# Kernel optimization log

Measured on AMD Instinct MI355X. Metric: run time of the kernel, lower is better.

Reference implementation:

```python
import jax, jax.numpy as jnp
import numpy as np
import math

N, E, D, H, L = 50000, 800000, 256, 8, 8
DK = D // H
DFF = 4 * D


def _layernorm(h, g, b, eps=1e-5):
    m = jnp.mean(h, axis=-1, keepdims=True)
    v = jnp.mean((h - m) ** 2, axis=-1, keepdims=True)
    return (h - m) * jax.lax.rsqrt(v + eps) * g + b


def setup_inputs() -> dict:
    key = jax.random.key(0)
    ks = jax.random.split(key, 16)
    s = 1.0 / math.sqrt(D)
    x = jax.random.normal(ks[0], (N, D), dtype=jnp.float32)
    # every node gets >=1 in-edge so z > 0 everywhere (as in real connected graphs)
    edge_src = jax.random.randint(ks[1], (E,), 0, N, dtype=jnp.int32)
    edge_dst = jnp.concatenate([
        jnp.arange(N, dtype=jnp.int32),
        jax.random.randint(ks[2], (E - N,), 0, N, dtype=jnp.int32),
    ])
    return {
        "x": x,
        "edge_src": edge_src,
        "edge_dst": edge_dst,
        "Wq": jax.random.normal(ks[3], (L, D, D), dtype=jnp.float32) * s,
        "bq": jnp.zeros((L, D), dtype=jnp.float32),
        "Wk": jax.random.normal(ks[4], (L, D, D), dtype=jnp.float32) * s,
        "Wv": jax.random.normal(ks[5], (L, D, D), dtype=jnp.float32) * s,
        "Wo": jax.random.normal(ks[6], (L, D, D), dtype=jnp.float32) * s,
        "bo": jnp.zeros((L, D), dtype=jnp.float32),
        "ln1_g": jnp.ones((L, D), dtype=jnp.float32),
        "ln1_b": jnp.zeros((L, D), dtype=jnp.float32),
        "W1": jax.random.normal(ks[7], (L, D, DFF), dtype=jnp.float32) * s,
        "b1": jnp.zeros((L, DFF), dtype=jnp.float32),
        "W2": jax.random.normal(ks[8], (L, DFF, D), dtype=jnp.float32) * (1.0 / math.sqrt(DFF)),
        "b2": jnp.zeros((L, D), dtype=jnp.float32),
        "ln2_g": jnp.ones((L, D), dtype=jnp.float32),
        "ln2_b": jnp.zeros((L, D), dtype=jnp.float32),
    }


def _layer(x, src, dst, Wq, bq, Wk, Wv, Wo, bo, g1, b1n, W1, b1, W2, b2, g2, b2n):
    n = x.shape[0]
    q = (x @ Wq + bq).reshape(n, H, DK)
    k = (x @ Wk).reshape(n, H, DK)
    v = (x @ Wv).reshape(n, H, DK)
    # edge score: src_dot_dst('k','q') -> [E, H]
    score = jnp.einsum('ehd,ehd->eh', k[src], q[dst])
    # scaled_exp: exp(clamp(score / sqrt(d_k), -5, 5))
    score = jnp.exp(jnp.clip(score / math.sqrt(DK), -5.0, 5.0))
    # u_mul_e + sum aggregation -> wv [N, H, DK]; copy_edge + sum -> z [N, H]
    msg = v[src] * score[:, :, None]
    wv = jax.ops.segment_sum(msg, dst, num_segments=n)
    z = jax.ops.segment_sum(score, dst, num_segments=n)
    o = (wv / z[:, :, None]).reshape(n, D)
    h = _layernorm(x + o @ Wo + bo, g1, b1n)
    # FFN with residual + layernorm
    ff = jax.nn.relu(h @ W1 + b1) @ W2 + b2
    return _layernorm(h + ff, g2, b2n)


def reference(x, edge_src, edge_dst, Wq, bq, Wk, Wv, Wo, bo, ln1_g, ln1_b,
              W1, b1, W2, b2, ln2_g, ln2_b):
    for i in range(L):
        x = _layer(x, edge_src, edge_dst, Wq[i], bq[i], Wk[i], Wv[i], Wo[i],
                   bo[i], ln1_g[i], ln1_b[i], W1[i], b1[i], W2[i], b2[i],
                   ln2_g[i], ln2_b[i])
    return x
```

## Files before the change

kernel.cpp:

```cpp
#include <hip/hip_runtime.h>
#include <cstdint>
#include <cstddef>

#define D 256
#define H 8
#define DFF 1024

typedef short s16x8 __attribute__((ext_vector_type(8)));
typedef float f32x4 __attribute__((ext_vector_type(4)));

static inline int cdiv(int a, int b) { return (a + b - 1) / b; }

__device__ inline uint16_t f2bf(float x) {
    unsigned u = __float_as_uint(x);
    u += 0x7FFFu + ((u >> 16) & 1u);
    return (uint16_t)(u >> 16);
}
__device__ inline float bf2f(uint16_t h) {
    return __uint_as_float(((unsigned)h) << 16);
}

__device__ inline void gload_lds16(const void* g, void* l) {
    __builtin_amdgcn_global_load_lds(
        (const __attribute__((address_space(1))) void*)g,
        (__attribute__((address_space(3))) void*)l, 16, 0, 0);
}

__global__ __launch_bounds__(256) void zero_int_kernel(int* __restrict__ p, int count)
{
    int i = blockIdx.x * blockDim.x + threadIdx.x;
    if (i < count) p[i] = 0;
}

__global__ __launch_bounds__(256) void count_deg_kernel(
    const int* __restrict__ edst, int* __restrict__ deg, int E)
{
    int e = blockIdx.x * blockDim.x + threadIdx.x;
    if (e < E) atomicAdd(&deg[edst[e]], 1);
}

__global__ __launch_bounds__(256) void block_sum_kernel(
    const int* __restrict__ deg, int* __restrict__ bsum, int N)
{
    int t = threadIdx.x;
    int gid = blockIdx.x * 256 + t;
    int val = (gid < N) ? deg[gid] : 0;
    #pragma unroll
    for (int o = 1; o < 64; o <<= 1) val += __shfl_xor(val, o);
    __shared__ int r[4];
    if ((t & 63) == 0) r[t >> 6] = val;
    __syncthreads();
    if (t == 0) bsum[blockIdx.x] = r[0] + r[1] + r[2] + r[3];
}

__global__ __launch_bounds__(256) void scan_bsum_kernel(int* __restrict__ bsum, int nb)
{
    __shared__ int tmp[256];
    int t = threadIdx.x;
    int val = (t < nb) ? bsum[t] : 0;
    tmp[t] = val;
    __syncthreads();
    for (int off = 1; off < 256; off <<= 1) {
        int add = (t >= off) ? tmp[t - off] : 0;
        __syncthreads();
        tmp[t] += add;
        __syncthreads();
    }
    if (t < nb) bsum[t] = tmp[t] - val;
}

__global__ __launch_bounds__(256) void scan_write_kernel(
    const int* __restrict__ deg, const int* __restrict__ bsum,
    int* __restrict__ rowptr, int* __restrict__ cursor, int N)
{
    __shared__ int tmp[256];
    int t = threadIdx.x;
    int gid = blockIdx.x * 256 + t;
    int val = (gid < N) ? deg[gid] : 0;
    tmp[t] = val;
    __syncthreads();
    for (int off = 1; off < 256; off <<= 1) {
        int add = (t >= off) ? tmp[t - off] : 0;
        __syncthreads();
        tmp[t] += add;
        __syncthreads();
    }
    int excl = tmp[t] - val + bsum[blockIdx.x];
    if (gid < N) { rowptr[gid] = excl; cursor[gid] = excl; }
    if (gid == N - 1) rowptr[N] = excl + val;
}

__global__ __launch_bounds__(256) void fill_csr_kernel(
    const int* __restrict__ esrc, const int* __restrict__ edst,
    int* __restrict__ cursor, int* __restrict__ csr_src, int E)
{
    int e = blockIdx.x * blockDim.x + threadIdx.x;
    if (e < E) {
        int pos = atomicAdd(&cursor[edst[e]], 1);
        csr_src[pos] = esrc[e];
    }
}

__global__ __launch_bounds__(256) void transpose_cast_kernel(
    const float* __restrict__ in, uint16_t* __restrict__ out,
    int R, int C, size_t inLS, size_t outLS)
{
    __shared__ float t[32][33];
    in  += blockIdx.z * inLS;
    out += blockIdx.z * outLS;
    int c0 = blockIdx.x * 32, r0 = blockIdx.y * 32;
    int tx = threadIdx.x, ty = threadIdx.y;
    #pragma unroll
    for (int i = 0; i < 4; ++i)
        t[ty + i * 8][tx] = in[(size_t)(r0 + ty + i * 8) * C + c0 + tx];
    __syncthreads();
    #pragma unroll
    for (int i = 0; i < 4; ++i)
        out[(size_t)(c0 + ty + i * 8) * R + r0 + tx] = f2bf(t[tx][ty + i * 8]);
}

__global__ __launch_bounds__(256) void cast_f32_bf16_kernel(
    const float* __restrict__ in, uint16_t* __restrict__ out, int n4)
{
    int i = blockIdx.x * blockDim.x + threadIdx.x;
    if (i >= n4) return;
    float4 f = ((const float4*)in)[i];
    uint16_t o0 = f2bf(f.x), o1 = f2bf(f.y), o2 = f2bf(f.z), o3 = f2bf(f.w);
    uint2 pk;
    pk.x = (unsigned)o0 | ((unsigned)o1 << 16);
    pk.y = (unsigned)o2 | ((unsigned)o3 << 16);
    ((uint2*)out)[i] = pk;
}

__global__ __launch_bounds__(256) void build_qkv_bias_kernel(
    const float* __restrict__ bq, float* __restrict__ qb, int total)
{
    int i = blockIdx.x * blockDim.x + threadIdx.x;
    if (i >= total) return;
    int l = i / 768, c = i - l * 768;
    qb[i] = (c < 256) ? bq[l * 256 + c] : 0.f;
}

__global__ __launch_bounds__(256) void gemm_bf16_kernel(
    const uint16_t* __restrict__ A, int lda, int M, int K,
    const uint16_t* __restrict__ BT, int Nc,
    const float* __restrict__ bias,
    uint16_t* __restrict__ Cb, int relu)
{
    __shared__ __align__(16) uint16_t As[128 * 32];
    __shared__ __align__(16) uint16_t Bs[128 * 32];

    const int tid  = threadIdx.x;
    const int lane = tid & 63;
    const int w    = tid >> 6;
    const int wr   = w >> 1, wc = w & 1;
    const int quad = lane >> 4;
    const int l15  = lane & 15;

    const int nwg = gridDim.x * gridDim.y;
    const int lin = blockIdx.y * gridDim.x + blockIdx.x;
    const int xcd = lin & 7, idx = lin >> 3;
    const int q8 = nwg >> 3, r8 = nwg & 7;
    const int lin2 = (xcd < r8 ? xcd * (q8 + 1) : r8 * (q8 + 1) + (xcd - r8) * q8) + idx;
    const int mt = lin2 % gridDim.x;
    const int nt = lin2 / gridDim.x;

    const int m0 = mt * 128;
    const int n0 = nt * 128;

    f32x4 acc[4][4] = {};

    const int jbase = w * 2;
    const int srow  = lane >> 2;
    const int skc   = (lane & 3) * 8;

    for (int k0 = 0; k0 < K; k0 += 32) {
        #pragma unroll
        for (int jj = 0; jj < 2; ++jj) {
            int j = jbase + jj;
            int r = j * 16 + srow;
            int gr = m0 + r; if (gr > M - 1) gr = M - 1;
            gload_lds16(A  + (size_t)gr * lda + k0 + skc, &As[j * 512]);
            gload_lds16(BT + (size_t)(n0 + r) * K + k0 + skc, &Bs[j * 512]);
        }
        __syncthreads();

        s16x8 af[4], bf[4];
        #pragma unroll
        for (int t = 0; t < 4; ++t) {
            af[t] = *(const s16x8*)&As[(wr * 64 + t * 16 + l15) * 32 + quad * 8];
            bf[t] = *(const s16x8*)&Bs[(wc * 64 + t * 16 + l15) * 32 + quad * 8];
        }
        #pragma unroll
        for (int i = 0; i < 4; ++i)
            #pragma unroll
            for (int jt = 0; jt < 4; ++jt)
                acc[i][jt] = __builtin_amdgcn_mfma_f32_16x16x32_bf16(
                    af[i], bf[jt], acc[i][jt], 0, 0, 0);
        __syncthreads();
    }

    float bv[4];
    #pragma unroll
    for (int jt = 0; jt < 4; ++jt)
        bv[jt] = bias ? bias[n0 + wc * 64 + jt * 16 + l15] : 0.f;

    #pragma unroll
    for (int i = 0; i < 4; ++i) {
        #pragma unroll
        for (int r = 0; r < 4; ++r) {
            int m = m0 + wr * 64 + i * 16 + quad * 4 + r;
            if (m >= M) continue;
            #pragma unroll
            for (int jt = 0; jt < 4; ++jt) {
                int n = n0 + wc * 64 + jt * 16 + l15;
                float val = acc[i][jt][r] + bv[jt];
                if (relu) val = fmaxf(val, 0.f);
                Cb[(size_t)m * Nc + n] = f2bf(val);
            }
        }
    }
}

__global__ __launch_bounds__(256) void gemm_ln_kernel(
    const uint16_t* __restrict__ A, int lda, int M, int K,
    const uint16_t* __restrict__ BT,
    const float* __restrict__ bias,
    const float* __restrict__ resid,
    const float* __restrict__ g, const float* __restrict__ b,
    float* __restrict__ Cf, uint16_t* __restrict__ Cb)
{
    __shared__ __align__(16) uint16_t As[64 * 32];
    __shared__ __align__(16) uint16_t Bs[256 * 32];
    __shared__ float sS[64][4];
    __shared__ float sQ[64][4];

    const int tid  = threadIdx.x;
    const int lane = tid & 63;
    const int w    = tid >> 6;
    const int quad = lane >> 4;
    const int l15  = lane & 15;

    const int m0 = blockIdx.x * 64;

    f32x4 acc[4][4] = {};

    for (int k0 = 0; k0 < K; k0 += 32) {
        {
            int slot = tid;
            int r = slot >> 2, kc = (slot & 3) * 8;
            int gr = m0 + r; if (gr > M - 1) gr = M - 1;
            gload_lds16(A + (size_t)gr * lda + k0 + kc, &As[slot * 8]);
        }
        #pragma unroll
        for (int i = 0; i < 4; ++i) {
            int slot = i * 256 + tid;
            int n = slot >> 2, kc = (slot & 3) * 8;
            gload_lds16(BT + (size_t)n * K + k0 + kc, &Bs[slot * 8]);
        }
        __syncthreads();

        s16x8 af[4], bf[4];
        #pragma unroll
        for (int t = 0; t < 4; ++t) {
            af[t] = *(const s16x8*)&As[(t * 16 + l15) * 32 + quad * 8];
            bf[t] = *(const s16x8*)&Bs[(w * 64 + t * 16 + l15) * 32 + quad * 8];
        }
        #pragma unroll
        for (int i = 0; i < 4; ++i)
            #pragma unroll
            for (int jt = 0; jt < 4; ++jt)
                acc[i][jt] = __builtin_amdgcn_mfma_f32_16x16x32_bf16(
                    af[i], bf[jt], acc[i][jt], 0, 0, 0);
        __syncthreads();
    }

    float bv[4], gv[4], bbv[4];
    #pragma unroll
    for (int jt = 0; jt < 4; ++jt) {
        int n = w * 64 + jt * 16 + l15;
        bv[jt]  = bias[n];
        gv[jt]  = g[n];
        bbv[jt] = b[n];
    }

    #pragma unroll
    for (int i = 0; i < 4; ++i) {
        #pragma unroll
        for (int r = 0; r < 4; ++r) {
            int ml = i * 16 + quad * 4 + r;
            int m  = m0 + ml;
            bool valid = (m < M);
            float s = 0.f, s2 = 0.f;
            #pragma unroll
            for (int jt = 0; jt < 4; ++jt) {
                int n = w * 64 + jt * 16 + l15;
                float val = acc[i][jt][r] + bv[jt];
                if (valid) val += resid[(size_t)m * 256 + n];
                acc[i][jt][r] = val;
                s += val;
                s2 += val * val;
            }
            #pragma unroll
            for (int o = 1; o < 16; o <<= 1) {
                s  += __shfl_xor(s, o);
                s2 += __shfl_xor(s2, o);
            }
            if (l15 == 0) { sS[ml][w] = s; sQ[ml][w] = s2; }
        }
    }
    __syncthreads();

    #pragma unroll
    for (int i = 0; i < 4; ++i) {
        #pragma unroll
        for (int r = 0; r < 4; ++r) {
            int ml = i * 16 + quad * 4 + r;
            int m  = m0 + ml;
            if (m >= M) continue;
            float s  = sS[ml][0] + sS[ml][1] + sS[ml][2] + sS[ml][3];
            float s2 = sQ[ml][0] + sQ[ml][1] + sQ[ml][2] + sQ[ml][3];
            float mean = s * (1.f / 256.f);
            float var  = s2 * (1.f / 256.f) - mean * mean;
            float rstd = rsqrtf(var + 1e-5f);
            #pragma unroll
            for (int jt = 0; jt < 4; ++jt) {
                int n = w * 64 + jt * 16 + l15;
                float out = (acc[i][jt][r] - mean) * rstd * gv[jt] + bbv[jt];
                Cf[(size_t)m * 256 + n] = out;
                if (Cb) Cb[(size_t)m * 256 + n] = f2bf(out);
            }
        }
    }
}

__global__ __launch_bounds__(256) void ffn_fused_kernel(
    const uint16_t* __restrict__ A,
    int M,
    const uint16_t* __restrict__ BT1,
    const float* __restrict__ b1,
    const uint16_t* __restrict__ BT2,
    const float* __restrict__ b2,
    const float* __restrict__ resid,
    const float* __restrict__ g, const float* __restrict__ b,
    float* __restrict__ Cf, uint16_t* __restrict__ Cb)
{
    __shared__ __align__(16) uint16_t As[64 * 32];
    __shared__ __align__(16) uint16_t Bs[256 * 32];
    __shared__ __align__(16) uint16_t Ts[64 * 128];
    __shared__ float sS[64][4];
    __shared__ float sQ[64][4];

    const int tid  = threadIdx.x;
    const int lane = tid & 63;
    const int w    = tid >> 6;
    const int quad = lane >> 4;
    const int l15  = lane & 15;
    const int m0   = blockIdx.x * 64;

    f32x4 acc2[4][4] = {};

    for (int c = 0; c < 8; ++c) {
        f32x4 acc1[4][2] = {};

        for (int k0 = 0; k0 < 256; k0 += 32) {
            {
                int r = tid >> 2, kc = (tid & 3) * 8;
                int gr = m0 + r; if (gr > M - 1) gr = M - 1;
                gload_lds16(A + (size_t)gr * 256 + k0 + kc, &As[tid * 8]);
            }
            #pragma unroll
            for (int i = 0; i < 2; ++i) {
                int slot = i * 256 + tid;
                int n = slot >> 2, kc = (slot & 3) * 8;
                gload_lds16(BT1 + (size_t)(c * 128 + n) * 256 + k0 + kc, &Bs[slot * 8]);
            }
            __syncthreads();

            s16x8 af[4], bf1[2];
            #pragma unroll
            for (int t = 0; t < 4; ++t)
                af[t] = *(const s16x8*)&As[(t * 16 + l15) * 32 + quad * 8];
            #pragma unroll
            for (int jt = 0; jt < 2; ++jt)
                bf1[jt] = *(const s16x8*)&Bs[(w * 32 + jt * 16 + l15) * 32 + quad * 8];
            #pragma unroll
            for (int i = 0; i < 4; ++i)
                #pragma unroll
                for (int jt = 0; jt < 2; ++jt)
                    acc1[i][jt] = __builtin_amdgcn_mfma_f32_16x16x32_bf16(
                        af[i], bf1[jt], acc1[i][jt], 0, 0, 0);
            __syncthreads();
        }

        float bv1[2];
        #pragma unroll
        for (int jt = 0; jt < 2; ++jt)
            bv1[jt] = b1[c * 128 + w * 32 + jt * 16 + l15];
        #pragma unroll
        for (int i = 0; i < 4; ++i)
            #pragma unroll
            for (int r = 0; r < 4; ++r) {
                int ml = i * 16 + quad * 4 + r;
                #pragma unroll
                for (int jt = 0; jt < 2; ++jt) {
                    float val = acc1[i][jt][r] + bv1[jt];
                    val = fmaxf(val, 0.f);
                    Ts[w * 2048 + ml * 32 + jt * 16 + l15] = f2bf(val);
                }
            }
        __syncthreads();

        for (int ts = 0; ts < 4; ++ts) {
            #pragma unroll
            for (int i = 0; i < 4; ++i) {
                int slot = i * 256 + tid;
                int n = slot >> 2, kc = (slot & 3) * 8;
                gload_lds16(BT2 + (size_t)n * 1024 + c * 128 + ts * 32 + kc, &Bs[slot * 8]);
            }
            __syncthreads();

            s16x8 af2[4], bf2[4];
            #pragma unroll
            for (int i = 0; i < 4; ++i)
                af2[i] = *(const s16x8*)&Ts[ts * 2048 + (i * 16 + l15) * 32 + quad * 8];
            #pragma unroll
            for (int jt = 0; jt < 4; ++jt)
                bf2[jt] = *(const s16x8*)&Bs[(w * 64 + jt * 16 + l15) * 32 + quad * 8];
            #pragma unroll
            for (int i = 0; i < 4; ++i)
                #pragma unroll
                for (int jt = 0; jt < 4; ++jt)
                    acc2[i][jt] = __builtin_amdgcn_mfma_f32_16x16x32_bf16(
                        af2[i], bf2[jt], acc2[i][jt], 0, 0, 0);
            __syncthreads();
        }
    }

    float bv[4], gv[4], bbv[4];
    #pragma unroll
    for (int jt = 0; jt < 4; ++jt) {
        int n = w * 64 + jt * 16 + l15;
        bv[jt]  = b2[n];
        gv[jt]  = g[n];
        bbv[jt] = b[n];
    }

    #pragma unroll
    for (int i = 0; i < 4; ++i) {
        #pragma unroll
        for (int r = 0; r < 4; ++r) {
            int ml = i * 16 + quad * 4 + r;
            int m  = m0 + ml;
            bool valid = (m < M);
            float s = 0.f, s2 = 0.f;
            #pragma unroll
            for (int jt = 0; jt < 4; ++jt) {
                int n = w * 64 + jt * 16 + l15;
                float val = acc2[i][jt][r] + bv[jt];
                if (valid) val += resid[(size_t)m * 256 + n];
                acc2[i][jt][r] = val;
                s += val;
                s2 += val * val;
            }
            #pragma unroll
            for (int o = 1; o < 16; o <<= 1) {
                s  += __shfl_xor(s, o);
                s2 += __shfl_xor(s2, o);
            }
            if (l15 == 0) { sS[ml][w] = s; sQ[ml][w] = s2; }
        }
    }
    __syncthreads();

    #pragma unroll
    for (int i = 0; i < 4; ++i) {
        #pragma unroll
        for (int r = 0; r < 4; ++r) {
            int ml = i * 16 + quad * 4 + r;
            int m  = m0 + ml;
            if (m >= M) continue;
            float s  = sS[ml][0] + sS[ml][1] + sS[ml][2] + sS[ml][3];
            float s2 = sQ[ml][0] + sQ[ml][1] + sQ[ml][2] + sQ[ml][3];
            float mean = s * (1.f / 256.f);
            float var  = s2 * (1.f / 256.f) - mean * mean;
            float rstd = rsqrtf(var + 1e-5f);
            #pragma unroll
            for (int jt = 0; jt < 4; ++jt) {
                int n = w * 64 + jt * 16 + l15;
                float out = (acc2[i][jt][r] - mean) * rstd * gv[jt] + bbv[jt];
                Cf[(size_t)m * 256 + n] = out;
                if (Cb) Cb[(size_t)m * 256 + n] = f2bf(out);
            }
        }
    }
}

__global__ __launch_bounds__(256) void node_attn_kernel(
    uint16_t* __restrict__ qkv,
    const int* __restrict__ rowptr, const int* __restrict__ csr_src, int N)
{
    int node = (blockIdx.x * blockDim.x + threadIdx.x) >> 6;
    int lane = threadIdx.x & 63;
    if (node >= N) return;

    uint16_t* qp = qkv + (size_t)node * 768 + lane * 4;
    uint2 qu = *(const uint2*)qp;
    float q0 = bf2f((uint16_t)(qu.x & 0xFFFF)), q1 = bf2f((uint16_t)(qu.x >> 16));
    float q2 = bf2f((uint16_t)(qu.y & 0xFFFF)), q3 = bf2f((uint16_t)(qu.y >> 16));

    float a0 = 0.f, a1 = 0.f, a2 = 0.f, a3 = 0.f, zacc = 0.f;
    const float inv_sqrt_dk = 0.17677669529663687f;

    int beg = rowptr[node], end = rowptr[node + 1];
    int i = beg;
    for (; i + 1 < end; i += 2) {
        int s0 = csr_src[i], s1 = csr_src[i + 1];
        const uint16_t* b0 = qkv + (size_t)s0 * 768;
        const uint16_t* b1 = qkv + (size_t)s1 * 768;
        uint2 ku0 = *(const uint2*)(b0 + 256 + lane * 4);
        uint2 ku1 = *(const uint2*)(b1 + 256 + lane * 4);
        uint2 vu0 = *(const uint2*)(b0 + 512 + lane * 4);
        uint2 vu1 = *(const uint2*)(b1 + 512 + lane * 4);

        float p0 = bf2f((uint16_t)(ku0.x & 0xFFFF)) * q0
                 + bf2f((uint16_t)(ku0.x >> 16))   * q1
                 + bf2f((uint16_t)(ku0.y & 0xFFFF)) * q2
                 + bf2f((uint16_t)(ku0.y >> 16))   * q3;
        float p1 = bf2f((uint16_t)(ku1.x & 0xFFFF)) * q0
                 + bf2f((uint16_t)(ku1.x >> 16))   * q1
                 + bf2f((uint16_t)(ku1.y & 0xFFFF)) * q2
                 + bf2f((uint16_t)(ku1.y >> 16))   * q3;
        p0 += __shfl_xor(p0, 1); p1 += __shfl_xor(p1, 1);
        p0 += __shfl_xor(p0, 2); p1 += __shfl_xor(p1, 2);
        p0 += __shfl_xor(p0, 4); p1 += __shfl_xor(p1, 4);
        float sc0 = __expf(fminf(fmaxf(p0 * inv_sqrt_dk, -5.f), 5.f));
        float sc1 = __expf(fminf(fmaxf(p1 * inv_sqrt_dk, -5.f), 5.f));

        a0 += bf2f((uint16_t)(vu0.x & 0xFFFF)) * sc0;
        a1 += bf2f((uint16_t)(vu0.x >> 16))   * sc0;
        a2 += bf2f((uint16_t)(vu0.y & 0xFFFF)) * sc0;
        a3 += bf2f((uint16_t)(vu0.y >> 16))   * sc0;
        zacc += sc0;
        a0 += bf2f((uint16_t)(vu1.x & 0xFFFF)) * sc1;
        a1 += bf2f((uint16_t)(vu1.x >> 16))   * sc1;
        a2 += bf2f((uint16_t)(vu1.y & 0xFFFF)) * sc1;
        a3 += bf2f((uint16_t)(vu1.y >> 16))   * sc1;
        zacc += sc1;
    }
    if (i < end) {
        int s = csr_src[i];
        const uint16_t* base = qkv + (size_t)s * 768;
        uint2 ku = *(const uint2*)(base + 256 + lane * 4);
        float p = bf2f((uint16_t)(ku.x & 0xFFFF)) * q0
                + bf2f((uint16_t)(ku.x >> 16))   * q1
                + bf2f((uint16_t)(ku.y & 0xFFFF)) * q2
                + bf2f((uint16_t)(ku.y >> 16))   * q3;
        p += __shfl_xor(p, 1);
        p += __shfl_xor(p, 2);
        p += __shfl_xor(p, 4);
        float sc = __expf(fminf(fmaxf(p * inv_sqrt_dk, -5.f), 5.f));
        uint2 vu = *(const uint2*)(base + 512 + lane * 4);
        a0 += bf2f((uint16_t)(vu.x & 0xFFFF)) * sc;
        a1 += bf2f((uint16_t)(vu.x >> 16))   * sc;
        a2 += bf2f((uint16_t)(vu.y & 0xFFFF)) * sc;
        a3 += bf2f((uint16_t)(vu.y >> 16))   * sc;
        zacc += sc;
    }
    float inv = 1.f / zacc;
    uint2 pk;
    pk.x = (unsigned)f2bf(a0 * inv) | ((unsigned)f2bf(a1 * inv) << 16);
    pk.y = (unsigned)f2bf(a2 * inv) | ((unsigned)f2bf(a3 * inv) << 16);
    *(uint2*)qp = pk;
}

extern "C" void kernel_launch(void* const* d_in, const int* in_sizes, int n_in,
                              void* d_out, int out_size, void* d_ws, size_t ws_size,
                              hipStream_t stream)
{
    const float* x0   = (const float*)d_in[0];
    const int* esrc   = (const int*)d_in[1];
    const int* edst   = (const int*)d_in[2];
    const float* Wq   = (const float*)d_in[3];
    const float* bq   = (const float*)d_in[4];
    const float* Wk   = (const float*)d_in[5];
    const float* Wv   = (const float*)d_in[6];
    const float* Wo   = (const float*)d_in[7];
    const float* bo   = (const float*)d_in[8];
    const float* ln1g = (const float*)d_in[9];
    const float* ln1b = (const float*)d_in[10];
    const float* W1   = (const float*)d_in[11];
    const float* b1   = (const float*)d_in[12];
    const float* W2   = (const float*)d_in[13];
    const float* b2   = (const float*)d_in[14];
    const float* ln2g = (const float*)d_in[15];
    const float* ln2b = (const float*)d_in[16];

    const int N = in_sizes[0] / D;
    const int E = in_sizes[1];
    const int L = in_sizes[3] / (D * D);
    const size_t ND = (size_t)N * D;

    char* p = (char*)d_ws;
    float* bufX = (float*)p;         p += ND * 4;
    uint16_t* xb  = (uint16_t*)p;
    uint16_t* t1  = xb;              p += ND * 2;
    uint16_t* qkv = (uint16_t*)p;    p += (size_t)N * 768 * 2;
    uint16_t* hb  = (uint16_t*)p;    p += ND * 2;
    uint16_t* BTqkv = (uint16_t*)p;  p += (size_t)L * 768 * 256 * 2;
    uint16_t* BTo   = (uint16_t*)p;  p += (size_t)L * 256 * 256 * 2;
    uint16_t* BT1   = (uint16_t*)p;  p += (size_t)L * 1024 * 256 * 2;
    uint16_t* BT2   = (uint16_t*)p;  p += (size_t)L * 256 * 1024 * 2;
    float* qbias    = (float*)p;     p += (size_t)L * 768 * 4;
    int* rowptr  = (int*)p;          p += (size_t)(N + 1) * 4;
    int* cursor  = (int*)p;          p += (size_t)N * 4;
    int* deg     = cursor;
    int* csr_src = (int*)p;          p += (size_t)E * 4;
    int* bsum    = (int*)p;
    (void)t1;

    const int nb = cdiv(N, 256);
    dim3 blk(256);
    int edgeBlocks = cdiv(E, 256);
    int nodeBlocks = cdiv(N, 4);

    dim3 tb(32, 8);
    transpose_cast_kernel<<<dim3(8, 8, L), tb, 0, stream>>>(Wq, BTqkv, 256, 256, (size_t)65536, (size_t)768 * 256);
    transpose_cast_kernel<<<dim3(8, 8, L), tb, 0, stream>>>(Wk, BTqkv + 256 * 256, 256, 256, (size_t)65536, (size_t)768 * 256);
    transpose_cast_kernel<<<dim3(8, 8, L), tb, 0, stream>>>(Wv, BTqkv + 512 * 256, 256, 256, (size_t)65536, (size_t)768 * 256);
    transpose_cast_kernel<<<dim3(8, 8, L), tb, 0, stream>>>(Wo, BTo, 256, 256, (size_t)65536, (size_t)65536);
    transpose_cast_kernel<<<dim3(32, 8, L), tb, 0, stream>>>(W1, BT1, 256, 1024, (size_t)262144, (size_t)262144);
    transpose_cast_kernel<<<dim3(8, 32, L), tb, 0, stream>>>(W2, BT2, 1024, 256, (size_t)262144, (size_t)262144);
    build_qkv_bias_kernel<<<cdiv(L * 768, 256), blk, 0, stream>>>(bq, qbias, L * 768);
    cast_f32_bf16_kernel<<<cdiv((int)(ND / 4), 256), blk, 0, stream>>>(x0, xb, (int)(ND / 4));

    zero_int_kernel<<<cdiv(N, 256), blk, 0, stream>>>(deg, N);
    count_deg_kernel<<<edgeBlocks, blk, 0, stream>>>(edst, deg, E);
    block_sum_kernel<<<nb, blk, 0, stream>>>(deg, bsum, N);
    scan_bsum_kernel<<<1, blk, 0, stream>>>(bsum, nb);
    scan_write_kernel<<<nb, blk, 0, stream>>>(deg, bsum, rowptr, cursor, N);
    fill_csr_kernel<<<edgeBlocks, blk, 0, stream>>>(esrc, edst, cursor, csr_src, E);

    const int Mt128 = cdiv(N, 128);
    const int Mt64  = cdiv(N, 64);
    dim3 gQKV(Mt128, 768 / 128);
    dim3 gLN(Mt64, 1);

    for (int l = 0; l < L; ++l) {
        const uint16_t* BTqkv_l = BTqkv + (size_t)l * 768 * 256;
        const uint16_t* BTo_l   = BTo + (size_t)l * 65536;
        const uint16_t* BT1_l   = BT1 + (size_t)l * 262144;
        const uint16_t* BT2_l   = BT2 + (size_t)l * 262144;
        const float* xin_f = (l == 0) ? x0 : bufX;

        gemm_bf16_kernel<<<gQKV, blk, 0, stream>>>(xb, 256, N, 256, BTqkv_l, 768,
            qbias + (size_t)l * 768, qkv, 0);

        node_attn_kernel<<<nodeBlocks, blk, 0, stream>>>(qkv, rowptr, csr_src, N);

        gemm_ln_kernel<<<gLN, blk, 0, stream>>>(qkv, 768, N, 256, BTo_l,
            bo + (size_t)l * 256, xin_f, ln1g + (size_t)l * 256, ln1b + (size_t)l * 256,
            bufX, hb);

        float* fout = (l == L - 1) ? (float*)d_out : bufX;
        ffn_fused_kernel<<<gLN, blk, 0, stream>>>(hb, N, BT1_l,
            b1 + (size_t)l * 1024, BT2_l, b2 + (size_t)l * 256, bufX,
            ln2g + (size_t)l * 256, ln2b + (size_t)l * 256,
            fout, (l == L - 1) ? nullptr : xb);

        xin_f = bufX;
    }
}
```

Measured before the change: 3.316 ms.

## Double-buffer LDS tiles in GEMM kernels with async prefetch and explicit waitcnt

The three MFMA GEMM kernels (qkv/FFN bf16 GEMM, GEMM+LayerNorm, fused FFN) now keep two LDS buffers and issue the global_load_lds for the next K-step before computing the current one. Explicit vmcnt waits and sched barriers replace the per-step syncthreads so loads overlap with MFMA work. The fused FFN kernel also packs its staging areas into a shared union and pads the intermediate tile to reduce bank conflicts, reusing that space for the LayerNorm reductions. This raises LDS use per block, which may lower occupancy, and relies on hand-counted vmcnt values being correct.

After: 3.131 ms. -5.6%, faster.

```diff
diff --git a/kernel.cpp b/kernel.cpp
--- a/kernel.cpp
+++ b/kernel.cpp
@@ -25,6 +25,14 @@
         (const __attribute__((address_space(1))) void*)g,
         (__attribute__((address_space(3))) void*)l, 16, 0, 0);
 }
+
+__device__ inline void vmcnt0() { asm volatile("s_waitcnt vmcnt(0)" ::: "memory"); }
+__device__ inline void vmcnt3() { asm volatile("s_waitcnt vmcnt(3)" ::: "memory"); }
+__device__ inline void vmcnt4() { asm volatile("s_waitcnt vmcnt(4)" ::: "memory"); }
+__device__ inline void vmcnt5() { asm volatile("s_waitcnt vmcnt(5)" ::: "memory"); }
+__device__ inline void lgkm0()  { asm volatile("s_waitcnt lgkmcnt(0)" ::: "memory"); }
+#define SB0() __builtin_amdgcn_sched_barrier(0)
+#define BARF() do { SB0(); __builtin_amdgcn_s_barrier(); SB0(); } while (0)
 
 __global__ __launch_bounds__(256) void zero_int_kernel(int* __restrict__ p, int count)
 {
@@ -147,8 +155,8 @@
     const float* __restrict__ bias,
     uint16_t* __restrict__ Cb, int relu)
 {
-    __shared__ __align__(16) uint16_t As[128 * 32];
-    __shared__ __align__(16) uint16_t Bs[128 * 32];
+    __shared__ __align__(16) uint16_t As[2][128 * 32];
+    __shared__ __align__(16) uint16_t Bs[2][128 * 32];
 
     const int tid  = threadIdx.x;
     const int lane = tid & 63;
@@ -174,22 +182,29 @@
     const int srow  = lane >> 2;
     const int skc   = (lane & 3) * 8;
 
-    for (int k0 = 0; k0 < K; k0 += 32) {
+    auto stage = [&](int b, int k0) {
         #pragma unroll
         for (int jj = 0; jj < 2; ++jj) {
             int j = jbase + jj;
             int r = j * 16 + srow;
             int gr = m0 + r; if (gr > M - 1) gr = M - 1;
-            gload_lds16(A  + (size_t)gr * lda + k0 + skc, &As[j * 512]);
-            gload_lds16(BT + (size_t)(n0 + r) * K + k0 + skc, &Bs[j * 512]);
-        }
-        __syncthreads();
-
+            gload_lds16(A  + (size_t)gr * lda + k0 + skc, &As[b][j * 512]);
+            gload_lds16(BT + (size_t)(n0 + r) * K + k0 + skc, &Bs[b][j * 512]);
+        }
+    };
+
+    const int nsteps = K >> 5;
+    stage(0, 0);
+    for (int s = 0; s < nsteps; ++s) {
+        if (s + 1 < nsteps) { stage((s + 1) & 1, (s + 1) << 5); vmcnt4(); }
+        else vmcnt0();
+        BARF();
+        const int b = s & 1;
         s16x8 af[4], bf[4];
         #pragma unroll
         for (int t = 0; t < 4; ++t) {
-            af[t] = *(const s16x8*)&As[(wr * 64 + t * 16 + l15) * 32 + quad * 8];
-            bf[t] = *(const s16x8*)&Bs[(wc * 64 + t * 16 + l15) * 32 + quad * 8];
+            af[t] = *(const s16x8*)&As[b][(wr * 64 + t * 16 + l15) * 32 + quad * 8];
+            bf[t] = *(const s16x8*)&Bs[b][(wc * 64 + t * 16 + l15) * 32 + quad * 8];
         }
         #pragma unroll
         for (int i = 0; i < 4; ++i)
@@ -197,7 +212,7 @@
             for (int jt = 0; jt < 4; ++jt)
                 acc[i][jt] = __builtin_amdgcn_mfma_f32_16x16x32_bf16(
                     af[i], bf[jt], acc[i][jt], 0, 0, 0);
-        __syncthreads();
+        BARF();
     }
 
     float bv[4];
@@ -230,8 +245,8 @@
     const float* __restrict__ g, const float* __restrict__ b,
     float* __restrict__ Cf, uint16_t* __restrict__ Cb)
 {
-    __shared__ __align__(16) uint16_t As[64 * 32];
-    __shared__ __align__(16) uint16_t Bs[256 * 32];
+    __shared__ __align__(16) uint16_t As[2][64 * 32];
+    __shared__ __align__(16) uint16_t Bs[2][256 * 32];
     __shared__ float sS[64][4];
     __shared__ float sQ[64][4];
 
@@ -245,26 +260,32 @@
 
     f32x4 acc[4][4] = {};
 
-    for (int k0 = 0; k0 < K; k0 += 32) {
+    auto stage = [&](int bb, int k0) {
         {
-            int slot = tid;
-            int r = slot >> 2, kc = (slot & 3) * 8;
+            int r = tid >> 2, kc = (tid & 3) * 8;
             int gr = m0 + r; if (gr > M - 1) gr = M - 1;
-            gload_lds16(A + (size_t)gr * lda + k0 + kc, &As[slot * 8]);
+            gload_lds16(A + (size_t)gr * lda + k0 + kc, &As[bb][tid * 8]);
         }
         #pragma unroll
         for (int i = 0; i < 4; ++i) {
             int slot = i * 256 + tid;
             int n = slot >> 2, kc = (slot & 3) * 8;
-            gload_lds16(BT + (size_t)n * K + k0 + kc, &Bs[slot * 8]);
-        }
-        __syncthreads();
-
+            gload_lds16(BT + (size_t)n * K + k0 + kc, &Bs[bb][slot * 8]);
+        }
+    };
+
+    const int nsteps = K >> 5;
+    stage(0, 0);
+    for (int s = 0; s < nsteps; ++s) {
+        if (s + 1 < nsteps) { stage((s + 1) & 1, (s + 1) << 5); vmcnt5(); }
+        else vmcnt0();
+        BARF();
+        const int bb = s & 1;
         s16x8 af[4], bf[4];
         #pragma unroll
         for (int t = 0; t < 4; ++t) {
-            af[t] = *(const s16x8*)&As[(t * 16 + l15) * 32 + quad * 8];
-            bf[t] = *(const s16x8*)&Bs[(w * 64 + t * 16 + l15) * 32 + quad * 8];
+            af[t] = *(const s16x8*)&As[bb][(t * 16 + l15) * 32 + quad * 8];
+            bf[t] = *(const s16x8*)&Bs[bb][(w * 64 + t * 16 + l15) * 32 + quad * 8];
         }
         #pragma unroll
         for (int i = 0; i < 4; ++i)
@@ -272,7 +293,7 @@
             for (int jt = 0; jt < 4; ++jt)
                 acc[i][jt] = __builtin_amdgcn_mfma_f32_16x16x32_bf16(
                     af[i], bf[jt], acc[i][jt], 0, 0, 0);
-        __syncthreads();
+        BARF();
     }
 
     float bv[4], gv[4], bbv[4];
@@ -345,11 +366,8 @@
     const float* __restrict__ g, const float* __restrict__ b,
     float* __restrict__ Cf, uint16_t* __restrict__ Cb)
 {
-    __shared__ __align__(16) uint16_t As[64 * 32];
-    __shared__ __align__(16) uint16_t Bs[256 * 32];
-    __shared__ __align__(16) uint16_t Ts[64 * 128];
-    __shared__ float sS[64][4];
-    __shared__ float sQ[64][4];
+    __shared__ __align__(16) uint16_t U[2][8192];
+    __shared__ __align__(16) uint16_t Ts[4][64][40];
 
     const int tid  = threadIdx.x;
     const int lane = tid & 63;
@@ -360,37 +378,53 @@
 
     f32x4 acc2[4][4] = {};
 
+    auto stage1 = [&](int bb, int c, int k0) {
+        {
+            int r = tid >> 2, kc = (tid & 3) * 8;
+            int gr = m0 + r; if (gr > M - 1) gr = M - 1;
+            gload_lds16(A + (size_t)gr * 256 + k0 + kc, &U[bb][tid * 8]);
+        }
+        #pragma unroll
+        for (int i = 0; i < 2; ++i) {
+            int slot = i * 256 + tid;
+            int n = slot >> 2, kc = (slot & 3) * 8;
+            gload_lds16(BT1 + (size_t)(c * 128 + n) * 256 + k0 + kc,
+                        &U[bb][2048 + slot * 8]);
+        }
+    };
+    auto stage2 = [&](int bb, int c, int ts) {
+        #pragma unroll
+        for (int i = 0; i < 4; ++i) {
+            int slot = i * 256 + tid;
+            int n = slot >> 2, kc = (slot & 3) * 8;
+            gload_lds16(BT2 + (size_t)n * 1024 + c * 128 + ts * 32 + kc,
+                        &U[bb][slot * 8]);
+        }
+    };
+
     for (int c = 0; c < 8; ++c) {
         f32x4 acc1[4][2] = {};
 
-        for (int k0 = 0; k0 < 256; k0 += 32) {
-            {
-                int r = tid >> 2, kc = (tid & 3) * 8;
-                int gr = m0 + r; if (gr > M - 1) gr = M - 1;
-                gload_lds16(A + (size_t)gr * 256 + k0 + kc, &As[tid * 8]);
-            }
-            #pragma unroll
-            for (int i = 0; i < 2; ++i) {
-                int slot = i * 256 + tid;
-                int n = slot >> 2, kc = (slot & 3) * 8;
-                gload_lds16(BT1 + (size_t)(c * 128 + n) * 256 + k0 + kc, &Bs[slot * 8]);
-            }
-            __syncthreads();
-
+        stage1(0, c, 0);
+        for (int ks = 0; ks < 8; ++ks) {
+            if (ks < 7) { stage1((ks + 1) & 1, c, (ks + 1) << 5); vmcnt3(); }
+            else vmcnt0();
+            BARF();
+            const int bb = ks & 1;
             s16x8 af[4], bf1[2];
             #pragma unroll
             for (int t = 0; t < 4; ++t)
-                af[t] = *(const s16x8*)&As[(t * 16 + l15) * 32 + quad * 8];
+                af[t] = *(const s16x8*)&U[bb][(t * 16 + l15) * 32 + quad * 8];
             #pragma unroll
             for (int jt = 0; jt < 2; ++jt)
-                bf1[jt] = *(const s16x8*)&Bs[(w * 32 + jt * 16 + l15) * 32 + quad * 8];
+                bf1[jt] = *(const s16x8*)&U[bb][2048 + (w * 32 + jt * 16 + l15) * 32 + quad * 8];
             #pragma unroll
             for (int i = 0; i < 4; ++i)
                 #pragma unroll
                 for (int jt = 0; jt < 2; ++jt)
                     acc1[i][jt] = __builtin_amdgcn_mfma_f32_16x16x32_bf16(
                         af[i], bf1[jt], acc1[i][jt], 0, 0, 0);
-            __syncthreads();
+            BARF();
         }
 
         float bv1[2];
@@ -406,36 +440,37 @@
                 for (int jt = 0; jt < 2; ++jt) {
                     float val = acc1[i][jt][r] + bv1[jt];
                     val = fmaxf(val, 0.f);
-                    Ts[w * 2048 + ml * 32 + jt * 16 + l15] = f2bf(val);
+                    Ts[w][ml][jt * 16 + l15] = f2bf(val);
                 }
             }
-        __syncthreads();
-
+        lgkm0();
+        BARF();
+
+        stage2(0, c, 0);
         for (int ts = 0; ts < 4; ++ts) {
-            #pragma unroll
-            for (int i = 0; i < 4; ++i) {
-                int slot = i * 256 + tid;
-                int n = slot >> 2, kc = (slot & 3) * 8;
-                gload_lds16(BT2 + (size_t)n * 1024 + c * 128 + ts * 32 + kc, &Bs[slot * 8]);
-            }
-            __syncthreads();
-
+            if (ts < 3) { stage2((ts + 1) & 1, c, ts + 1); vmcnt4(); }
+            else vmcnt0();
+            BARF();
+            const int bb = ts & 1;
             s16x8 af2[4], bf2[4];
             #pragma unroll
             for (int i = 0; i < 4; ++i)
-                af2[i] = *(const s16x8*)&Ts[ts * 2048 + (i * 16 + l15) * 32 + quad * 8];
+                af2[i] = *(const s16x8*)&Ts[ts][i * 16 + l15][quad * 8];
             #pragma unroll
             for (int jt = 0; jt < 4; ++jt)
-                bf2[jt] = *(const s16x8*)&Bs[(w * 64 + jt * 16 + l15) * 32 + quad * 8];
+                bf2[jt] = *(const s16x8*)&U[bb][(w * 64 + jt * 16 + l15) * 32 + quad * 8];
             #pragma unroll
             for (int i = 0; i < 4; ++i)
                 #pragma unroll
                 for (int jt = 0; jt < 4; ++jt)
                     acc2[i][jt] = __builtin_amdgcn_mfma_f32_16x16x32_bf16(
                         af2[i], bf2[jt], acc2[i][jt], 0, 0, 0);
-            __syncthreads();
-        }
-    }
+            BARF();
+        }
+    }
+
+    float* sS = (float*)&U[0][0];
+    float* sQ = (float*)&U[0][512];
 
     float bv[4], gv[4], bbv[4];
     #pragma unroll
@@ -456,9 +491,8 @@
             float s = 0.f, s2 = 0.f;
             #pragma unroll
             for (int jt = 0; jt < 4; ++jt) {
-                int n = w * 64 + jt * 16 + l15;
                 float val = acc2[i][jt][r] + bv[jt];
-                if (valid) val += resid[(size_t)m * 256 + n];
+                if (valid) val += resid[(size_t)m * 256 + w * 64 + jt * 16 + l15];
                 acc2[i][jt][r] = val;
                 s += val;
                 s2 += val * val;
@@ -468,7 +502,7 @@
                 s  += __shfl_xor(s, o);
                 s2 += __shfl_xor(s2, o);
             }
-            if (l15 == 0) { sS[ml][w] = s; sQ[ml][w] = s2; }
+            if (l15 == 0) { sS[ml * 4 + w] = s; sQ[ml * 4 + w] = s2; }
         }
     }
     __syncthreads();
@@ -480,8 +514,8 @@
             int ml = i * 16 + quad * 4 + r;
             int m  = m0 + ml;
             if (m >= M) continue;
-            float s  = sS[ml][0] + sS[ml][1] + sS[ml][2] + sS[ml][3];
-            float s2 = sQ[ml][0] + sQ[ml][1] + sQ[ml][2] + sQ[ml][3];
+            float s  = sS[ml * 4 + 0] + sS[ml * 4 + 1] + sS[ml * 4 + 2] + sS[ml * 4 + 3];
+            float s2 = sQ[ml * 4 + 0] + sQ[ml * 4 + 1] + sQ[ml * 4 + 2] + sQ[ml * 4 + 3];
             float mean = s * (1.f / 256.f);
             float var  = s2 * (1.f / 256.f) - mean * mean;
             float rstd = rsqrtf(var + 1e-5f);
@@ -603,8 +637,7 @@
 
     char* p = (char*)d_ws;
     float* bufX = (float*)p;         p += ND * 4;
-    uint16_t* xb  = (uint16_t*)p;
-    uint16_t* t1  = xb;              p += ND * 2;
+    uint16_t* xb  = (uint16_t*)p;    p += ND * 2;
     uint16_t* qkv = (uint16_t*)p;    p += (size_t)N * 768 * 2;
     uint16_t* hb  = (uint16_t*)p;    p += ND * 2;
     uint16_t* BTqkv = (uint16_t*)p;  p += (size_t)L * 768 * 256 * 2;
@@ -617,7 +650,6 @@
     int* deg     = cursor;
     int* csr_src = (int*)p;          p += (size_t)E * 4;
     int* bsum    = (int*)p;
-    (void)t1;
 
     const int nb = cdiv(N, 256);
     dim3 blk(256);
```
